# Optimization experiments

Measured on AMD Instinct MI355X. Metric: run time of the kernel, lower is better.

## Reference

```python
import jax, jax.numpy as jnp
import numpy as np
from jax import lax

EPS = 1e-5
NEG_SLOPE = 0.1
RES_SCALE = float(np.sqrt(0.5))


def upsample2x(x):
    # bilinear, align_corners=False (half-pixel), matches torch nn.Upsample(mode='bilinear')
    B, C, H, W = x.shape
    return jax.image.resize(x, (B, C, 2 * H, 2 * W), method='bilinear')


def modulated_conv2d(x, weight, styles, eps=EPS):
    # x: [B, I, H, W]; weight: [O, I, kh, kw]; styles: [B, I]
    B, I, H, W = x.shape
    O, _, kh, kw = weight.shape
    wmod = weight[None] * styles[:, None, :, None, None]            # [B,O,I,kh,kw]
    demod = lax.rsqrt(jnp.sum(wmod * wmod, axis=(2, 3, 4)) + eps)   # [B,O]
    wmod = wmod * demod[:, :, None, None, None]
    x_g = x.reshape(1, B * I, H, W)
    w_g = wmod.reshape(B * O, I, kh, kw)
    out = lax.conv_general_dilated(
        x_g, w_g, window_strides=(1, 1), padding=[(1, 1), (1, 1)],
        feature_group_count=B,
        dimension_numbers=('NCHW', 'OIHW', 'NCHW'))
    return out.reshape(B, O, H, W)


def style_block(x, w, n, conv_w, A_w, A_b, B_w, B_b, upsample):
    if upsample:
        x = upsample2x(x)
    scores = w @ A_w.T + A_b                      # [B, in_ch]
    x = modulated_conv2d(x, conv_w, scores)
    noise = n @ B_w.T + B_b                        # [B, out_ch]
    x = x + noise[:, :, None, None]
    return jnp.where(x >= 0, x, NEG_SLOPE * x)     # LeakyReLU(0.1)


def setup_inputs() -> dict:
    key = jax.random.key(0)
    ks = jax.random.split(key, 16)
    Bn, Ci, Co, Wd, Nd, H = 8, 256, 128, 512, 512, 64
    s = lambda k, shape, scale=0.05: jax.random.normal(k, shape, jnp.float32) * scale
    return {
        'x': jax.random.normal(ks[0], (Bn, Ci, H, H), jnp.float32),
        'w': jax.random.normal(ks[1], (Bn, Wd), jnp.float32),
        'n': jax.random.normal(ks[2], (Bn, Nd), jnp.float32),
        'rgb': jax.random.normal(ks[3], (Bn, 3, H, H), jnp.float32),
        'conv1_w': s(ks[4], (Ci, Ci, 3, 3)),
        'A1_w': s(ks[5], (Ci, Wd)), 'A1_b': jnp.ones((Ci,), jnp.float32),
        'B1_w': s(ks[6], (Ci, Nd)), 'B1_b': jnp.zeros((Ci,), jnp.float32),
        'conv2_w': s(ks[7], (Co, Ci, 3, 3)),
        'A2_w': s(ks[8], (Ci, Wd)), 'A2_b': jnp.ones((Ci,), jnp.float32),
        'B2_w': s(ks[9], (Co, Nd)), 'B2_b': jnp.zeros((Co,), jnp.float32),
        'rgb_w': s(ks[10], (3, Co, 1, 1)),
        'rgb_b': jnp.zeros((3,), jnp.float32),
    }


def reference(x, w, n, rgb, conv1_w, A1_w, A1_b, B1_w, B1_b,
              conv2_w, A2_w, A2_b, B2_w, B2_b, rgb_w, rgb_b):
    x = style_block(x, w, n, conv1_w, A1_w, A1_b, B1_w, B1_b, upsample=False)
    x = style_block(x, w, n, conv2_w, A2_w, A2_b, B2_w, B2_b, upsample=True)
    to_rgb = lax.conv_general_dilated(
        x, rgb_w, (1, 1), padding=[(0, 0), (0, 0)],
        dimension_numbers=('NCHW', 'OIHW', 'NCHW')) + rgb_b[None, :, None, None]
    rgb_out = (to_rgb + upsample2x(rgb)) * RES_SCALE
    return x, rgb_out
```

## Files before the change

### kernel.cpp

```cpp
#include <hip/hip_runtime.h>
#include <math.h>

#define BN 8
#define C1 256
#define C2 128
#define WD 512

typedef float  f32x4  __attribute__((ext_vector_type(4)));
typedef short  bf16x8 __attribute__((ext_vector_type(8)));
typedef unsigned short ushort_t;
typedef ushort_t us8 __attribute__((ext_vector_type(8)));
typedef ushort_t us4 __attribute__((ext_vector_type(4)));

__device__ __forceinline__ int clampi(int v, int lo, int hi) {
    return v < lo ? lo : (v > hi ? hi : v);
}
__device__ __forceinline__ float bf2f(ushort_t u) {
    return __uint_as_float(((unsigned int)u) << 16);
}
__device__ __forceinline__ ushort_t f2bf(float f) {
    unsigned int u = __float_as_uint(f);
    u = (u + 0x7fff + ((u >> 16) & 1)) >> 16;
    return (ushort_t)u;
}

__global__ __launch_bounds__(256)
void affine_kernel(const float* __restrict__ w, const float* __restrict__ n,
                   const float* __restrict__ A1w, const float* __restrict__ A1b,
                   const float* __restrict__ B1w, const float* __restrict__ B1b,
                   const float* __restrict__ A2w, const float* __restrict__ A2b,
                   const float* __restrict__ B2w, const float* __restrict__ B2b,
                   float* __restrict__ s1, float* __restrict__ s2,
                   float* __restrict__ n1, float* __restrict__ n2) {
    int tid = threadIdx.x;
    int gw = blockIdx.x * 4 + (tid >> 6);
    int lane = tid & 63;
    if (gw >= BN * 896) return;
    int b = gw / 896;
    int j = gw % 896;
    const float* vec; const float* M; const float* bias; float* out; int o;
    if (j < 256)      { o = j;       vec = w + b * WD; M = A1w; bias = A1b; out = s1 + b * 256; }
    else if (j < 512) { o = j - 256; vec = w + b * WD; M = A2w; bias = A2b; out = s2 + b * 256; }
    else if (j < 768) { o = j - 512; vec = n + b * WD; M = B1w; bias = B1b; out = n1 + b * 256; }
    else              { o = j - 768; vec = n + b * WD; M = B2w; bias = B2b; out = n2 + b * 128; }
    const float* row = M + (size_t)o * WD;
    int k0 = lane * 8;
    float4 v0 = *(const float4*)(vec + k0), v1 = *(const float4*)(vec + k0 + 4);
    float4 r0 = *(const float4*)(row + k0), r1 = *(const float4*)(row + k0 + 4);
    float acc = v0.x*r0.x + v0.y*r0.y + v0.z*r0.z + v0.w*r0.w
              + v1.x*r1.x + v1.y*r1.y + v1.z*r1.z + v1.w*r1.w;
    #pragma unroll
    for (int m = 1; m < 64; m <<= 1) acc += __shfl_xor(acc, m, 64);
    if (lane == 0) out[o] = acc + bias[o];
}

__global__ __launch_bounds__(256)
void demod_kernel(const float* __restrict__ cw1, const float* __restrict__ cw2,
                  const float* __restrict__ s1, const float* __restrict__ s2,
                  float* __restrict__ d1, float* __restrict__ d2) {
    int tid = threadIdx.x;
    int gw = blockIdx.x * 4 + (tid >> 6);
    int lane = tid & 63;
    if (gw >= BN * 384) return;
    int b = gw / 384;
    int j = gw % 384;
    const float* wbase; const float* s; float* dout; int o;
    if (j < 256) { o = j;       wbase = cw1; s = s1 + b * 256; dout = d1 + b * 256; }
    else         { o = j - 256; wbase = cw2; s = s2 + b * 256; dout = d2 + b * 128; }
    float acc = 0.f;
    #pragma unroll
    for (int i = 0; i < 4; i++) {
        int ic = lane * 4 + i;
        float sv = s[ic]; sv *= sv;
        const float* wk = wbase + ((size_t)o * 256 + ic) * 9;
        float t = 0.f;
        #pragma unroll
        for (int k = 0; k < 9; k++) t += wk[k] * wk[k];
        acc += t * sv;
    }
    #pragma unroll
    for (int m = 1; m < 64; m <<= 1) acc += __shfl_xor(acc, m, 64);
    if (lane == 0) dout[o] = rsqrtf(acc + 1e-5f);
}

__global__ __launch_bounds__(256)
void wprep_kernel(const float* __restrict__ cw1, const float* __restrict__ cw2,
                  ushort_t* __restrict__ wT1, ushort_t* __restrict__ wT2) {
    int idx = blockIdx.x * 256 + threadIdx.x;
    if (idx < 9 * 256 * 256) {
        int tap = idx >> 16;
        int oc = (idx >> 8) & 255;
        int ic = idx & 255;
        wT1[idx] = f2bf(cw1[((size_t)(oc * 256 + ic)) * 9 + tap]);
    } else if (idx < 9 * 256 * 256 + 9 * 128 * 256) {
        int e = idx - 9 * 256 * 256;
        int tap = e >> 15;
        int oc = (e >> 8) & 127;
        int ic = e & 255;
        wT2[e] = f2bf(cw2[((size_t)(oc * 256 + ic)) * 9 + tap]);
    }
}

__global__ __launch_bounds__(512)
void xprep_kernel(const float* __restrict__ x, const float* __restrict__ s1,
                  ushort_t* __restrict__ xTp) {
    int tid = threadIdx.x;
    int b = blockIdx.y;
    int px_lin = blockIdx.x * 16 + (tid >> 5);
    int ic8 = tid & 31;
    int gy = px_lin >> 6, gx = px_lin & 63;
    const float* xb = x + (((size_t)b * C1) << 12) + (gy << 6) + gx;
    float4 slo = *(const float4*)(s1 + b * 256 + ic8 * 8);
    float4 shi = *(const float4*)(s1 + b * 256 + ic8 * 8 + 4);
    float sv[8] = {slo.x, slo.y, slo.z, slo.w, shi.x, shi.y, shi.z, shi.w};
    us8 h;
    #pragma unroll
    for (int j = 0; j < 8; j++) {
        float v = xb[((size_t)(ic8 * 8 + j)) << 12];
        h[j] = f2bf(v * sv[j]);
    }
    *(us8*)(xTp + (size_t)b * 66 * 66 * 256 + ((size_t)(gy + 1) * 66 + gx + 1) * 256 + ic8 * 8) = h;
}

__global__ __launch_bounds__(256)
void upsample_kernel(const ushort_t* __restrict__ y1T, const float* __restrict__ s2,
                     ushort_t* __restrict__ y1up) {
    int flat = blockIdx.x * 256 + threadIdx.x;
    int b = blockIdx.y;
    int ic8 = flat & 31;
    int pxl = flat >> 5;
    int ux = pxl & 127, uy = pxl >> 7;
    int jyA; float wyA;
    if (uy & 1) { jyA = uy >> 1;       wyA = 0.75f; }
    else        { jyA = (uy >> 1) - 1; wyA = 0.25f; }
    int jxA; float wxA;
    if (ux & 1) { jxA = ux >> 1;       wxA = 0.75f; }
    else        { jxA = (ux >> 1) - 1; wxA = 0.25f; }
    int yA = clampi(jyA, 0, 63), yB = clampi(jyA + 1, 0, 63);
    int xA = clampi(jxA, 0, 63), xB = clampi(jxA + 1, 0, 63);
    float wyB = 1.f - wyA, wxB = 1.f - wxA;
    const ushort_t* yb = y1T + (size_t)b * 64 * 64 * 256 + ic8 * 8;
    us8 qAA = *(const us8*)(yb + (size_t)(yA * 64 + xA) * 256);
    us8 qAB = *(const us8*)(yb + (size_t)(yA * 64 + xB) * 256);
    us8 qBA = *(const us8*)(yb + (size_t)(yB * 64 + xA) * 256);
    us8 qBB = *(const us8*)(yb + (size_t)(yB * 64 + xB) * 256);
    float4 slo = *(const float4*)(s2 + b * 256 + ic8 * 8);
    float4 shi = *(const float4*)(s2 + b * 256 + ic8 * 8 + 4);
    float sv[8] = {slo.x, slo.y, slo.z, slo.w, shi.x, shi.y, shi.z, shi.w};
    us8 h;
    #pragma unroll
    for (int j = 0; j < 8; j++) {
        float v = wyA * (wxA * bf2f(qAA[j]) + wxB * bf2f(qAB[j]))
                + wyB * (wxA * bf2f(qBA[j]) + wxB * bf2f(qBB[j]));
        h[j] = f2bf(v * sv[j]);
    }
    *(us8*)(y1up + (size_t)b * 130 * 130 * 256 + ((size_t)(uy + 1) * 130 + ux + 1) * 256 + ic8 * 8) = h;
}

template<int ROWSTR, int OCTOT, int OUTW, int TPR, bool IS_CONV2>
__global__ __launch_bounds__(256, 2)
void conv_mfma(const ushort_t* __restrict__ inp, const ushort_t* __restrict__ wT,
               const float* __restrict__ dmod, const float* __restrict__ nza,
               ushort_t* __restrict__ outT,
               const float* __restrict__ rgb_in, const float* __restrict__ rw,
               const float* __restrict__ rb, float* __restrict__ xout,
               float* __restrict__ rgbo) {
    __shared__ __align__(16) ushort_t actS[18 * 18 * 32];
    __shared__ __align__(16) ushort_t wS[9 * 64 * 32];
    int b = blockIdx.z, ocg = blockIdx.y, tile = blockIdx.x;
    int tyT = tile / TPR, txT = tile % TPR;
    int ty0 = tyT * 16, tx0 = txT * 16;
    int tid = threadIdx.x, lane = tid & 63, wave = tid >> 6;
    int col = lane & 15, quad = lane >> 4;

    const ushort_t* inb = inp + (size_t)b * ROWSTR * ROWSTR * 256;

    int actOff[6]; bool actOk[6];
    #pragma unroll
    for (int i = 0; i < 6; i++) {
        int u = tid + 256 * i;
        actOk[i] = (u < 1296);
        int pxl = u >> 2, ic8 = u & 3;
        int py = pxl / 18, px = pxl - py * 18;
        actOff[i] = ((ty0 + py) * ROWSTR + tx0 + px) * 256 + ic8 * 8;
    }
    int wOff[9];
    #pragma unroll
    for (int i = 0; i < 9; i++) {
        int u = tid + 256 * i;
        int tap = u >> 8, oc = (u >> 2) & 63, ic8 = u & 3;
        wOff[i] = (tap * OCTOT + ocg * 64 + oc) * 256 + ic8 * 8;
    }

    us8 aReg[6], wReg[9];
#define LOADK(KC) { \
    _Pragma("unroll") for (int i = 0; i < 6; i++) \
        if (actOk[i]) aReg[i] = *(const us8*)(inb + actOff[i] + (KC) * 32); \
    _Pragma("unroll") for (int i = 0; i < 9; i++) \
        wReg[i] = *(const us8*)(wT + wOff[i] + (KC) * 32); }
#define STOREK() { \
    _Pragma("unroll") for (int i = 0; i < 6; i++) \
        if (actOk[i]) *(us8*)(actS + (size_t)(tid + 256 * i) * 8) = aReg[i]; \
    _Pragma("unroll") for (int i = 0; i < 9; i++) \
        *(us8*)(wS + (size_t)(tid + 256 * i) * 8) = wReg[i]; }

    f32x4 acc[4][4];
    #pragma unroll
    for (int mt = 0; mt < 4; mt++)
        #pragma unroll
        for (int nt = 0; nt < 4; nt++) acc[mt][nt] = (f32x4)(0.f);

    LOADK(0);
    STOREK();
    __syncthreads();

    for (int kc = 0; kc < 8; kc++) {
        if (kc < 7) LOADK(kc + 1);
        #pragma unroll
        for (int tap = 0; tap < 9; tap++) {
            const int dy = tap / 3, dx = tap % 3;
            bf16x8 a[4], bb[4];
            #pragma unroll
            for (int mt = 0; mt < 4; mt++)
                a[mt] = *(const bf16x8*)(wS + ((tap * 64 + mt * 16 + col) * 32 + quad * 8));
            #pragma unroll
            for (int nt = 0; nt < 4; nt++)
                bb[nt] = *(const bf16x8*)(actS + (((4 * wave + nt + dy) * 18 + col + dx) * 32 + quad * 8));
            #pragma unroll
            for (int mt = 0; mt < 4; mt++)
                #pragma unroll
                for (int nt = 0; nt < 4; nt++)
                    acc[mt][nt] = __builtin_amdgcn_mfma_f32_16x16x32_bf16(a[mt], bb[nt], acc[mt][nt], 0, 0, 0);
        }
        __syncthreads();
        if (kc < 7) { STOREK(); }
        __syncthreads();
    }
#undef LOADK
#undef STOREK

    if (!IS_CONV2) {
        #pragma unroll
        for (int mt = 0; mt < 4; mt++) {
            int oc0 = ocg * 64 + mt * 16 + quad * 4;
            float4 dv = *(const float4*)(dmod + b * OCTOT + oc0);
            float4 nv = *(const float4*)(nza + b * OCTOT + oc0);
            float dva[4] = {dv.x, dv.y, dv.z, dv.w};
            float nva[4] = {nv.x, nv.y, nv.z, nv.w};
            #pragma unroll
            for (int nt = 0; nt < 4; nt++) {
                int gy = ty0 + 4 * wave + nt, gx = tx0 + col;
                us4 h;
                #pragma unroll
                for (int r = 0; r < 4; r++) {
                    float t = acc[mt][nt][r] * dva[r] + nva[r];
                    t = (t >= 0.f) ? t : 0.1f * t;
                    h[r] = f2bf(t);
                }
                *(us4*)(outT + ((size_t)b * OUTW * OUTW + gy * OUTW + gx) * 256 + oc0) = h;
            }
        }
    } else {
        float dva[4][4], nva[4][4], rwa[3][4][4];
        #pragma unroll
        for (int mt = 0; mt < 4; mt++) {
            int oc0 = ocg * 64 + mt * 16 + quad * 4;
            float4 dv = *(const float4*)(dmod + b * 128 + oc0);
            float4 nv = *(const float4*)(nza + b * 128 + oc0);
            dva[mt][0] = dv.x; dva[mt][1] = dv.y; dva[mt][2] = dv.z; dva[mt][3] = dv.w;
            nva[mt][0] = nv.x; nva[mt][1] = nv.y; nva[mt][2] = nv.z; nva[mt][3] = nv.w;
            #pragma unroll
            for (int c = 0; c < 3; c++) {
                float4 rv = *(const float4*)(rw + c * 128 + oc0);
                rwa[c][mt][0] = rv.x; rwa[c][mt][1] = rv.y; rwa[c][mt][2] = rv.z; rwa[c][mt][3] = rv.w;
            }
        }
        #pragma unroll
        for (int nt = 0; nt < 4; nt++) {
            int uy = ty0 + 4 * wave + nt, ux = tx0 + col;
            float pc0 = 0.f, pc1 = 0.f, pc2 = 0.f;
            #pragma unroll
            for (int mt = 0; mt < 4; mt++) {
                int oc0 = ocg * 64 + mt * 16 + quad * 4;
                #pragma unroll
                for (int r = 0; r < 4; r++) {
                    float t = acc[mt][nt][r] * dva[mt][r] + nva[mt][r];
                    t = (t >= 0.f) ? t : 0.1f * t;
                    xout[(((size_t)b * 128 + oc0 + r) << 14) + (uy << 7) + ux] = t;
                    pc0 += rwa[0][mt][r] * t;
                    pc1 += rwa[1][mt][r] * t;
                    pc2 += rwa[2][mt][r] * t;
                }
            }
            if (ocg == 0 && quad == 0) {
                int jyA; float wyA;
                if (uy & 1) { jyA = uy >> 1;       wyA = 0.75f; }
                else        { jyA = (uy >> 1) - 1; wyA = 0.25f; }
                int jxA; float wxA;
                if (ux & 1) { jxA = ux >> 1;       wxA = 0.75f; }
                else        { jxA = (ux >> 1) - 1; wxA = 0.25f; }
                int yA = clampi(jyA, 0, 63), yB = clampi(jyA + 1, 0, 63);
                int xA = clampi(jxA, 0, 63), xB = clampi(jxA + 1, 0, 63);
                float wyB = 1.f - wyA, wxB = 1.f - wxA;
                const float* rp3 = rgb_in + (((size_t)b * 3) << 12);
                float up[3];
                #pragma unroll
                for (int c = 0; c < 3; c++) {
                    const float* rc = rp3 + ((size_t)c << 12);
                    up[c] = wyA * (wxA * rc[(yA << 6) + xA] + wxB * rc[(yA << 6) + xB])
                          + wyB * (wxA * rc[(yB << 6) + xA] + wxB * rc[(yB << 6) + xB]);
                }
                pc0 += rb[0] + up[0];
                pc1 += rb[1] + up[1];
                pc2 += rb[2] + up[2];
            }
            const float S = 0.70710678118654752f;
            atomicAdd(rgbo + (((size_t)b * 3 + 0) << 14) + (uy << 7) + ux, pc0 * S);
            atomicAdd(rgbo + (((size_t)b * 3 + 1) << 14) + (uy << 7) + ux, pc1 * S);
            atomicAdd(rgbo + (((size_t)b * 3 + 2) << 14) + (uy << 7) + ux, pc2 * S);
        }
    }
}

extern "C" void kernel_launch(void* const* d_in, const int* in_sizes, int n_in,
                              void* d_out, int out_size, void* d_ws, size_t ws_size,
                              hipStream_t stream) {
    (void)in_sizes; (void)n_in; (void)out_size; (void)ws_size;
    const float* x     = (const float*)d_in[0];
    const float* w     = (const float*)d_in[1];
    const float* n     = (const float*)d_in[2];
    const float* rgb   = (const float*)d_in[3];
    const float* cw1   = (const float*)d_in[4];
    const float* A1w   = (const float*)d_in[5];
    const float* A1b   = (const float*)d_in[6];
    const float* B1w   = (const float*)d_in[7];
    const float* B1b   = (const float*)d_in[8];
    const float* cw2   = (const float*)d_in[9];
    const float* A2w   = (const float*)d_in[10];
    const float* A2b   = (const float*)d_in[11];
    const float* B2w   = (const float*)d_in[12];
    const float* B2b   = (const float*)d_in[13];
    const float* rgbw  = (const float*)d_in[14];
    const float* rgbb  = (const float*)d_in[15];

    char* ws = (char*)d_ws;
    float* s1 = (float*)(ws);
    float* s2 = (float*)(ws + 8192);
    float* d1 = (float*)(ws + 16384);
    float* d2 = (float*)(ws + 24576);
    float* n1 = (float*)(ws + 28672);
    float* n2 = (float*)(ws + 36864);
    ushort_t* wT1  = (ushort_t*)(ws + 40960);
    ushort_t* wT2  = (ushort_t*)(ws + 1220608);
    ushort_t* xTp  = (ushort_t*)(ws + 1810432);
    ushort_t* y1up = (ushort_t*)(ws + 19652608);
    ushort_t* y1T  = (ushort_t*)(ws + 88875008);

    float* xout = (float*)d_out;
    float* rgbo = xout + (size_t)BN * C2 * 128 * 128;

    hipMemsetAsync(xTp, 0, 17842176 + 69222400, stream);
    hipMemsetAsync(rgbo, 0, (size_t)BN * 3 * 128 * 128 * 4, stream);

    affine_kernel<<<1792, 256, 0, stream>>>(w, n, A1w, A1b, B1w, B1b, A2w, A2b, B2w, B2b,
                                            s1, s2, n1, n2);
    demod_kernel<<<768, 256, 0, stream>>>(cw1, cw2, s1, s2, d1, d2);
    wprep_kernel<<<(9 * 256 * 256 + 9 * 128 * 256 + 255) / 256, 256, 0, stream>>>(cw1, cw2, wT1, wT2);
    xprep_kernel<<<dim3(256, BN), 512, 0, stream>>>(x, s1, xTp);
    conv_mfma<66, 256, 64, 4, false><<<dim3(16, 4, BN), 256, 0, stream>>>(
        xTp, wT1, d1, n1, y1T, nullptr, nullptr, nullptr, nullptr, nullptr);
    upsample_kernel<<<dim3(2048, BN), 256, 0, stream>>>(y1T, s2, y1up);
    conv_mfma<130, 128, 128, 8, true><<<dim3(64, 2, BN), 256, 0, stream>>>(
        y1up, wT2, d2, n2, nullptr, rgb, rgbw, rgbb, xout, rgbo);
}
```

Before: 318.3 us.

## Drop padded buffers, relayout weights and LDS, reuse activation fragments across taps

Removes the zero-padded activation buffers and their large memset, handling borders in the conv loader with predicated zero fills instead. Weights are re-laid out per 32-channel K chunk so each chunk is contiguous, and LDS is split per quad-of-8-channels to reduce bank conflicts. The tap loop is restructured to load six activation rows once per dx and reuse them across dy, the conv1 epilogue stages output through LDS for coalesced 16-byte stores, and the RGB partials are reduced across quads before atomics so only a quarter of lanes issue atomics. This adds more index arithmetic and an extra barrier in the epilogue.

```diff
diff --git a/kernel.cpp b/kernel.cpp
--- a/kernel.cpp
+++ b/kernel.cpp
@@ -87,16 +87,20 @@
 void wprep_kernel(const float* __restrict__ cw1, const float* __restrict__ cw2,
                   ushort_t* __restrict__ wT1, ushort_t* __restrict__ wT2) {
     int idx = blockIdx.x * 256 + threadIdx.x;
-    if (idx < 9 * 256 * 256) {
-        int tap = idx >> 16;
-        int oc = (idx >> 8) & 255;
-        int ic = idx & 255;
+    if (idx < 8 * 9 * 256 * 32) {
+        int icw = idx & 31;
+        int r = idx >> 5;
+        int oc = r & 255; r >>= 8;
+        int tap = r % 9, kc = r / 9;
+        int ic = kc * 32 + icw;
         wT1[idx] = f2bf(cw1[((size_t)(oc * 256 + ic)) * 9 + tap]);
-    } else if (idx < 9 * 256 * 256 + 9 * 128 * 256) {
-        int e = idx - 9 * 256 * 256;
-        int tap = e >> 15;
-        int oc = (e >> 8) & 127;
-        int ic = e & 255;
+    } else if (idx < 589824 + 8 * 9 * 128 * 32) {
+        int e = idx - 589824;
+        int icw = e & 31;
+        int r = e >> 5;
+        int oc = r & 127; r >>= 7;
+        int tap = r % 9, kc = r / 9;
+        int ic = kc * 32 + icw;
         wT2[e] = f2bf(cw2[((size_t)(oc * 256 + ic)) * 9 + tap]);
     }
 }
@@ -108,8 +112,7 @@
     int b = blockIdx.y;
     int px_lin = blockIdx.x * 16 + (tid >> 5);
     int ic8 = tid & 31;
-    int gy = px_lin >> 6, gx = px_lin & 63;
-    const float* xb = x + (((size_t)b * C1) << 12) + (gy << 6) + gx;
+    const float* xb = x + (((size_t)b * C1) << 12) + px_lin;
     float4 slo = *(const float4*)(s1 + b * 256 + ic8 * 8);
     float4 shi = *(const float4*)(s1 + b * 256 + ic8 * 8 + 4);
     float sv[8] = {slo.x, slo.y, slo.z, slo.w, shi.x, shi.y, shi.z, shi.w};
@@ -119,7 +122,7 @@
         float v = xb[((size_t)(ic8 * 8 + j)) << 12];
         h[j] = f2bf(v * sv[j]);
     }
-    *(us8*)(xTp + (size_t)b * 66 * 66 * 256 + ((size_t)(gy + 1) * 66 + gx + 1) * 256 + ic8 * 8) = h;
+    *(us8*)(xTp + ((size_t)b << 20) + (size_t)px_lin * 256 + ic8 * 8) = h;
 }
 
 __global__ __launch_bounds__(256)
@@ -139,7 +142,7 @@
     int yA = clampi(jyA, 0, 63), yB = clampi(jyA + 1, 0, 63);
     int xA = clampi(jxA, 0, 63), xB = clampi(jxA + 1, 0, 63);
     float wyB = 1.f - wyA, wxB = 1.f - wxA;
-    const ushort_t* yb = y1T + (size_t)b * 64 * 64 * 256 + ic8 * 8;
+    const ushort_t* yb = y1T + (((size_t)b) << 20) + ic8 * 8;
     us8 qAA = *(const us8*)(yb + (size_t)(yA * 64 + xA) * 256);
     us8 qAB = *(const us8*)(yb + (size_t)(yA * 64 + xB) * 256);
     us8 qBA = *(const us8*)(yb + (size_t)(yB * 64 + xA) * 256);
@@ -154,10 +157,10 @@
                 + wyB * (wxA * bf2f(qBA[j]) + wxB * bf2f(qBB[j]));
         h[j] = f2bf(v * sv[j]);
     }
-    *(us8*)(y1up + (size_t)b * 130 * 130 * 256 + ((size_t)(uy + 1) * 130 + ux + 1) * 256 + ic8 * 8) = h;
-}
-
-template<int ROWSTR, int OCTOT, int OUTW, int TPR, bool IS_CONV2>
+    *(us8*)(y1up + ((size_t)b << 22) + (size_t)(uy * 128 + ux) * 256 + ic8 * 8) = h;
+}
+
+template<int IW, int OCTOT, int TPR, bool IS_CONV2>
 __global__ __launch_bounds__(256, 2)
 void conv_mfma(const ushort_t* __restrict__ inp, const ushort_t* __restrict__ wT,
                const float* __restrict__ dmod, const float* __restrict__ nza,
@@ -165,44 +168,52 @@
                const float* __restrict__ rgb_in, const float* __restrict__ rw,
                const float* __restrict__ rb, float* __restrict__ xout,
                float* __restrict__ rgbo) {
-    __shared__ __align__(16) ushort_t actS[18 * 18 * 32];
-    __shared__ __align__(16) ushort_t wS[9 * 64 * 32];
-    int b = blockIdx.z, ocg = blockIdx.y, tile = blockIdx.x;
-    int tyT = tile / TPR, txT = tile % TPR;
-    int ty0 = tyT * 16, tx0 = txT * 16;
-    int tid = threadIdx.x, lane = tid & 63, wave = tid >> 6;
-    int col = lane & 15, quad = lane >> 4;
-
-    const ushort_t* inb = inp + (size_t)b * ROWSTR * ROWSTR * 256;
+    __shared__ __align__(16) ushort_t smem[28928];
+    ushort_t* actS = smem;
+    ushort_t* wS   = smem + 10432;
+
+    const int b = blockIdx.z, ocg = blockIdx.y, tile = blockIdx.x;
+    const int tyT = tile / TPR, txT = tile % TPR;
+    const int ty0 = tyT * 16, tx0 = txT * 16;
+    const int tid = threadIdx.x, lane = tid & 63, wave = tid >> 6;
+    const int col = lane & 15, quad = lane >> 4;
+
+    const ushort_t* inb = inp + (size_t)b * IW * IW * 256;
 
     int actOff[6]; bool actOk[6];
     #pragma unroll
     for (int i = 0; i < 6; i++) {
         int u = tid + 256 * i;
-        actOk[i] = (u < 1296);
-        int pxl = u >> 2, ic8 = u & 3;
-        int py = pxl / 18, px = pxl - py * 18;
-        actOff[i] = ((ty0 + py) * ROWSTR + tx0 + px) * 256 + ic8 * 8;
+        int px_l = u >> 2, q = u & 3;
+        int py = px_l / 18, pxx = px_l - py * 18;
+        int gy = ty0 + py - 1, gx = tx0 + pxx - 1;
+        bool ok = (u < 1296) && (gy >= 0) && (gy < IW) && (gx >= 0) && (gx < IW);
+        actOk[i] = ok;
+        actOff[i] = ok ? ((gy * IW + gx) * 256 + q * 8) : 0;
     }
     int wOff[9];
     #pragma unroll
     for (int i = 0; i < 9; i++) {
         int u = tid + 256 * i;
-        int tap = u >> 8, oc = (u >> 2) & 63, ic8 = u & 3;
-        wOff[i] = (tap * OCTOT + ocg * 64 + oc) * 256 + ic8 * 8;
-    }
+        int tap = u >> 8, oc = (u >> 2) & 63, q = u & 3;
+        wOff[i] = (tap * OCTOT + ocg * 64 + oc) * 32 + q * 8;
+    }
+    const int KSTRIDE = 9 * OCTOT * 32;
 
     us8 aReg[6], wReg[9];
+    const us8 zer = (us8)0;
 #define LOADK(KC) { \
     _Pragma("unroll") for (int i = 0; i < 6; i++) \
-        if (actOk[i]) aReg[i] = *(const us8*)(inb + actOff[i] + (KC) * 32); \
+        aReg[i] = actOk[i] ? *(const us8*)(inb + actOff[i] + (KC) * 32) : zer; \
     _Pragma("unroll") for (int i = 0; i < 9; i++) \
-        wReg[i] = *(const us8*)(wT + wOff[i] + (KC) * 32); }
+        wReg[i] = *(const us8*)(wT + wOff[i] + (KC) * KSTRIDE); }
 #define STOREK() { \
-    _Pragma("unroll") for (int i = 0; i < 6; i++) \
-        if (actOk[i]) *(us8*)(actS + (size_t)(tid + 256 * i) * 8) = aReg[i]; \
-    _Pragma("unroll") for (int i = 0; i < 9; i++) \
-        *(us8*)(wS + (size_t)(tid + 256 * i) * 8) = wReg[i]; }
+    _Pragma("unroll") for (int i = 0; i < 6; i++) { \
+        int u = tid + 256 * i; \
+        if (u < 1296) *(us8*)(actS + (u & 3) * 2608 + (u >> 2) * 8) = aReg[i]; } \
+    _Pragma("unroll") for (int i = 0; i < 9; i++) { \
+        int u = tid + 256 * i; \
+        *(us8*)(wS + (u & 3) * 4624 + (u >> 2) * 8) = wReg[i]; } }
 
     f32x4 acc[4][4];
     #pragma unroll
@@ -214,23 +225,31 @@
     STOREK();
     __syncthreads();
 
+    const ushort_t* bbase = actS + quad * 2608 + (72 * wave + col) * 8;
+    const ushort_t* abase = wS + quad * 4624 + col * 8;
+
     for (int kc = 0; kc < 8; kc++) {
         if (kc < 7) LOADK(kc + 1);
         #pragma unroll
-        for (int tap = 0; tap < 9; tap++) {
-            const int dy = tap / 3, dx = tap % 3;
-            bf16x8 a[4], bb[4];
+        for (int dx = 0; dx < 3; dx++) {
+            bf16x8 bb[6];
             #pragma unroll
-            for (int mt = 0; mt < 4; mt++)
-                a[mt] = *(const bf16x8*)(wS + ((tap * 64 + mt * 16 + col) * 32 + quad * 8));
+            for (int r = 0; r < 6; r++)
+                bb[r] = *(const bf16x8*)(bbase + (r * 18 + dx) * 8);
             #pragma unroll
-            for (int nt = 0; nt < 4; nt++)
-                bb[nt] = *(const bf16x8*)(actS + (((4 * wave + nt + dy) * 18 + col + dx) * 32 + quad * 8));
-            #pragma unroll
-            for (int mt = 0; mt < 4; mt++)
+            for (int dy = 0; dy < 3; dy++) {
+                const int tap = dy * 3 + dx;
+                bf16x8 a[4];
                 #pragma unroll
-                for (int nt = 0; nt < 4; nt++)
-                    acc[mt][nt] = __builtin_amdgcn_mfma_f32_16x16x32_bf16(a[mt], bb[nt], acc[mt][nt], 0, 0, 0);
+                for (int mt = 0; mt < 4; mt++)
+                    a[mt] = *(const bf16x8*)(abase + (tap * 64 + mt * 16) * 8);
+                #pragma unroll
+                for (int mt = 0; mt < 4; mt++)
+                    #pragma unroll
+                    for (int nt = 0; nt < 4; nt++)
+                        acc[mt][nt] = __builtin_amdgcn_mfma_f32_16x16x32_bf16(
+                            a[mt], bb[nt + dy], acc[mt][nt], 0, 0, 0);
+            }
         }
         __syncthreads();
         if (kc < 7) { STOREK(); }
@@ -239,7 +258,8 @@
 #undef LOADK
 #undef STOREK
 
-    if (!IS_CONV2) {
+    if constexpr (!IS_CONV2) {
+        ushort_t* oS = smem;
         #pragma unroll
         for (int mt = 0; mt < 4; mt++) {
             int oc0 = ocg * 64 + mt * 16 + quad * 4;
@@ -249,7 +269,7 @@
             float nva[4] = {nv.x, nv.y, nv.z, nv.w};
             #pragma unroll
             for (int nt = 0; nt < 4; nt++) {
-                int gy = ty0 + 4 * wave + nt, gx = tx0 + col;
+                int px = (4 * wave + nt) * 16 + col;
                 us4 h;
                 #pragma unroll
                 for (int r = 0; r < 4; r++) {
@@ -257,8 +277,17 @@
                     t = (t >= 0.f) ? t : 0.1f * t;
                     h[r] = f2bf(t);
                 }
-                *(us4*)(outT + ((size_t)b * OUTW * OUTW + gy * OUTW + gx) * 256 + oc0) = h;
+                *(us4*)(oS + px * 80 + mt * 16 + quad * 4) = h;
             }
+        }
+        __syncthreads();
+        #pragma unroll
+        for (int p = 0; p < 8; p++) {
+            int idx = tid + 256 * p;
+            int px = idx >> 3, oc8 = idx & 7;
+            us8 v = *(const us8*)(oS + px * 80 + oc8 * 8);
+            int gy = ty0 + (px >> 4), gx = tx0 + (px & 15);
+            *(us8*)(outT + ((size_t)b * IW * IW + gy * IW + gx) * 256 + ocg * 64 + oc8 * 8) = v;
         }
     } else {
         float dva[4][4], nva[4][4], rwa[3][4][4];
@@ -292,32 +321,36 @@
                     pc2 += rwa[2][mt][r] * t;
                 }
             }
-            if (ocg == 0 && quad == 0) {
-                int jyA; float wyA;
-                if (uy & 1) { jyA = uy >> 1;       wyA = 0.75f; }
-                else        { jyA = (uy >> 1) - 1; wyA = 0.25f; }
-                int jxA; float wxA;
-                if (ux & 1) { jxA = ux >> 1;       wxA = 0.75f; }
-                else        { jxA = (ux >> 1) - 1; wxA = 0.25f; }
-                int yA = clampi(jyA, 0, 63), yB = clampi(jyA + 1, 0, 63);
-                int xA = clampi(jxA, 0, 63), xB = clampi(jxA + 1, 0, 63);
-                float wyB = 1.f - wyA, wxB = 1.f - wxA;
-                const float* rp3 = rgb_in + (((size_t)b * 3) << 12);
-                float up[3];
-                #pragma unroll
-                for (int c = 0; c < 3; c++) {
-                    const float* rc = rp3 + ((size_t)c << 12);
-                    up[c] = wyA * (wxA * rc[(yA << 6) + xA] + wxB * rc[(yA << 6) + xB])
-                          + wyB * (wxA * rc[(yB << 6) + xA] + wxB * rc[(yB << 6) + xB]);
+            pc0 += __shfl_xor(pc0, 16, 64); pc0 += __shfl_xor(pc0, 32, 64);
+            pc1 += __shfl_xor(pc1, 16, 64); pc1 += __shfl_xor(pc1, 32, 64);
+            pc2 += __shfl_xor(pc2, 16, 64); pc2 += __shfl_xor(pc2, 32, 64);
+            if (quad == 0) {
+                if (ocg == 0) {
+                    int jyA; float wyA;
+                    if (uy & 1) { jyA = uy >> 1;       wyA = 0.75f; }
+                    else        { jyA = (uy >> 1) - 1; wyA = 0.25f; }
+                    int jxA; float wxA;
+                    if (ux & 1) { jxA = ux >> 1;       wxA = 0.75f; }
+                    else        { jxA = (ux >> 1) - 1; wxA = 0.25f; }
+                    int yA = clampi(jyA, 0, 63), yB = clampi(jyA + 1, 0, 63);
+                    int xA = clampi(jxA, 0, 63), xB = clampi(jxA + 1, 0, 63);
+                    float wyB = 1.f - wyA, wxB = 1.f - wxA;
+                    const float* rp3 = rgb_in + (((size_t)b * 3) << 12);
+                    #pragma unroll
+                    for (int c = 0; c < 3; c++) {
+                        const float* rc = rp3 + ((size_t)c << 12);
+                        float up = wyA * (wxA * rc[(yA << 6) + xA] + wxB * rc[(yA << 6) + xB])
+                                 + wyB * (wxA * rc[(yB << 6) + xA] + wxB * rc[(yB << 6) + xB]);
+                        if (c == 0) pc0 += rb[0] + up;
+                        else if (c == 1) pc1 += rb[1] + up;
+                        else pc2 += rb[2] + up;
+                    }
                 }
-                pc0 += rb[0] + up[0];
-                pc1 += rb[1] + up[1];
-                pc2 += rb[2] + up[2];
+                const float S = 0.70710678118654752f;
+                atomicAdd(rgbo + (((size_t)b * 3 + 0) << 14) + (uy << 7) + ux, pc0 * S);
+                atomicAdd(rgbo + (((size_t)b * 3 + 1) << 14) + (uy << 7) + ux, pc1 * S);
+                atomicAdd(rgbo + (((size_t)b * 3 + 2) << 14) + (uy << 7) + ux, pc2 * S);
             }
-            const float S = 0.70710678118654752f;
-            atomicAdd(rgbo + (((size_t)b * 3 + 0) << 14) + (uy << 7) + ux, pc0 * S);
-            atomicAdd(rgbo + (((size_t)b * 3 + 1) << 14) + (uy << 7) + ux, pc1 * S);
-            atomicAdd(rgbo + (((size_t)b * 3 + 2) << 14) + (uy << 7) + ux, pc2 * S);
         }
     }
 }
@@ -353,23 +386,22 @@
     ushort_t* wT1  = (ushort_t*)(ws + 40960);
     ushort_t* wT2  = (ushort_t*)(ws + 1220608);
     ushort_t* xTp  = (ushort_t*)(ws + 1810432);
-    ushort_t* y1up = (ushort_t*)(ws + 19652608);
-    ushort_t* y1T  = (ushort_t*)(ws + 88875008);
+    ushort_t* y1up = (ushort_t*)(ws + 18587648);
+    ushort_t* y1T  = (ushort_t*)(ws + 85696512);
 
     float* xout = (float*)d_out;
     float* rgbo = xout + (size_t)BN * C2 * 128 * 128;
 
-    hipMemsetAsync(xTp, 0, 17842176 + 69222400, stream);
     hipMemsetAsync(rgbo, 0, (size_t)BN * 3 * 128 * 128 * 4, stream);
 
     affine_kernel<<<1792, 256, 0, stream>>>(w, n, A1w, A1b, B1w, B1b, A2w, A2b, B2w, B2b,
                                             s1, s2, n1, n2);
     demod_kernel<<<768, 256, 0, stream>>>(cw1, cw2, s1, s2, d1, d2);
-    wprep_kernel<<<(9 * 256 * 256 + 9 * 128 * 256 + 255) / 256, 256, 0, stream>>>(cw1, cw2, wT1, wT2);
+    wprep_kernel<<<(589824 + 294912) / 256, 256, 0, stream>>>(cw1, cw2, wT1, wT2);
     xprep_kernel<<<dim3(256, BN), 512, 0, stream>>>(x, s1, xTp);
-    conv_mfma<66, 256, 64, 4, false><<<dim3(16, 4, BN), 256, 0, stream>>>(
+    conv_mfma<64, 256, 4, false><<<dim3(16, 4, BN), 256, 0, stream>>>(
         xTp, wT1, d1, n1, y1T, nullptr, nullptr, nullptr, nullptr, nullptr);
     upsample_kernel<<<dim3(2048, BN), 256, 0, stream>>>(y1T, s2, y1up);
-    conv_mfma<130, 128, 128, 8, true><<<dim3(64, 2, BN), 256, 0, stream>>>(
+    conv_mfma<128, 128, 8, true><<<dim3(64, 2, BN), 256, 0, stream>>>(
         y1up, wT2, d2, n2, nullptr, rgb, rgbw, rgbb, xout, rgbo);
 }
```

Measured after the change: 274.1 us. 1.16x faster.
